# Kernel tuning notes

Hardware: AMD Instinct MI355X
Metric: run time of the kernel (lower is better)

Reference implementation:

```python
import jax, jax.numpy as jnp
import numpy as np

N_NODES = 50000
N_EDGES = 800000
N_GRAPHS = 64
IN_CH = 128
HID = 128
PROC_X = 128
Q_DIM = 768
PROC_Q = 128
OUT_CH = 32


def setup_inputs() -> dict:
    key = jax.random.key(0)
    ks = jax.random.split(key, 16)
    inp = {
        "x": jax.random.normal(ks[0], (N_NODES, IN_CH), dtype=jnp.float32),
        "edge_index": jax.random.randint(ks[1], (2, N_EDGES), 0, N_NODES, dtype=jnp.int64),
        "batch": jnp.sort(jax.random.randint(ks[2], (N_NODES,), 0, N_GRAPHS, dtype=jnp.int64)),
        "question_embedding": jax.random.normal(ks[3], (N_GRAPHS, Q_DIM), dtype=jnp.float32),
    }
    s = 1.0 / np.sqrt(HID)
    inp["W0"] = jax.random.uniform(ks[4], (IN_CH, HID), minval=-s, maxval=s)
    inp["b0"] = jnp.zeros((HID,), jnp.float32)
    inp["W1"] = jax.random.uniform(ks[5], (HID, HID), minval=-s, maxval=s)
    inp["b1"] = jnp.zeros((HID,), jnp.float32)
    inp["W2"] = jax.random.uniform(ks[6], (HID, PROC_X), minval=-s, maxval=s)
    inp["b2"] = jnp.zeros((PROC_X,), jnp.float32)
    inp["fc0_w"] = jax.random.uniform(ks[7], (Q_DIM, PROC_Q), minval=-s, maxval=s)
    inp["fc0_b"] = jnp.zeros((PROC_Q,), jnp.float32)
    inp["fc1_w"] = jax.random.uniform(ks[8], (PROC_X + PROC_Q, HID), minval=-s, maxval=s)
    inp["fc1_b"] = jnp.zeros((HID,), jnp.float32)
    inp["fc2_w"] = jax.random.uniform(ks[9], (HID, OUT_CH), minval=-s, maxval=s)
    inp["fc2_b"] = jnp.zeros((OUT_CH,), jnp.float32)
    return inp


def _gcn_norm(edge_index, n_nodes):
    """Add self-loops and compute symmetric GCN normalization per edge."""
    loop = jnp.arange(n_nodes, dtype=edge_index.dtype)
    src = jnp.concatenate([edge_index[0], loop])
    dst = jnp.concatenate([edge_index[1], loop])
    ones = jnp.ones_like(dst, dtype=jnp.float32)
    deg = jax.ops.segment_sum(ones, dst, num_segments=n_nodes)
    dinv = jnp.where(deg > 0, jax.lax.rsqrt(deg), 0.0)
    norm = dinv[src] * dinv[dst]  # [E+N]
    return src, dst, norm


def _gcn_conv(x, src, dst, norm, W, b):
    h = x @ W                                # [N, F_out]
    msg = h[src] * norm[:, None]             # gather + scale  [E+N, F_out]
    agg = jax.ops.segment_sum(msg, dst, num_segments=x.shape[0])
    return agg + b


def reference(x, edge_index, batch, question_embedding,
              W0, b0, W1, b1, W2, b2,
              fc0_w, fc0_b, fc1_w, fc1_b, fc2_w, fc2_b):
    n = x.shape[0]
    src, dst, norm = _gcn_norm(edge_index, n)
    h = jax.nn.relu(_gcn_conv(x, src, dst, norm, W0, b0))
    h = jax.nn.relu(_gcn_conv(h, src, dst, norm, W1, b1))
    h = jax.nn.relu(_gcn_conv(h, src, dst, norm, W2, b2))
    q = jax.nn.relu(question_embedding @ fc0_w + fc0_b)  # [G, PROC_Q]
    q_exp = q[batch]                                      # [N, PROC_Q]
    combined = jnp.concatenate([h, q_exp], axis=1)
    out = jax.nn.relu(combined @ fc1_w + fc1_b)
    out = out @ fc2_w + fc2_b
    return out
```

## Files before the change

### kernel.cpp

```cpp
#include <hip/hip_runtime.h>
#include <hip/hip_bf16.h>

#define N_NODES 50000
#define N_EDGES 800000
#define N_GRAPHS 64
#define LSTR 136

typedef __attribute__((ext_vector_type(4))) short s4v;
typedef __attribute__((ext_vector_type(8))) short s8v;
typedef __attribute__((ext_vector_type(16))) float f16v;

struct HL { short hi, lo; };

__device__ inline HL bsplit(float f) {
    HL r;
    unsigned u = __float_as_uint(f);
    unsigned rh = (u + 0x7FFFu + ((u >> 16) & 1u)) >> 16;
    r.hi = (short)rh;
    float fh = __uint_as_float(rh << 16);
    float fl = f - fh;
    unsigned u2 = __float_as_uint(fl);
    unsigned rl = (u2 + 0x7FFFu + ((u2 >> 16) & 1u)) >> 16;
    r.lo = (short)rl;
    return r;
}

__device__ inline unsigned short f2bf(float f) {
    unsigned u = __float_as_uint(f);
    return (unsigned short)((u + 0x7FFFu + ((u >> 16) & 1u)) >> 16);
}

__device__ inline float bflo(unsigned u) { return __uint_as_float(u << 16); }
__device__ inline float bfhi(unsigned u) { return __uint_as_float(u & 0xFFFF0000u); }

__device__ inline void gat8(const unsigned* __restrict__ Hs,
                            const unsigned short* __restrict__ colA,
                            int e, int l, float& a0, float& a1) {
    uint4 cw = *(const uint4*)(colA + e);
    unsigned u0 = Hs[(cw.x & 0xFFFFu) * 64u + l];
    unsigned u1 = Hs[(cw.x >> 16) * 64u + l];
    unsigned u2 = Hs[(cw.y & 0xFFFFu) * 64u + l];
    unsigned u3 = Hs[(cw.y >> 16) * 64u + l];
    unsigned u4 = Hs[(cw.z & 0xFFFFu) * 64u + l];
    unsigned u5 = Hs[(cw.z >> 16) * 64u + l];
    unsigned u6 = Hs[(cw.w & 0xFFFFu) * 64u + l];
    unsigned u7 = Hs[(cw.w >> 16) * 64u + l];
    a0 += ((bflo(u0) + bflo(u1)) + (bflo(u2) + bflo(u3)))
        + ((bflo(u4) + bflo(u5)) + (bflo(u6) + bflo(u7)));
    a1 += ((bfhi(u0) + bfhi(u1)) + (bfhi(u2) + bfhi(u3)))
        + ((bfhi(u4) + bfhi(u5)) + (bfhi(u6) + bfhi(u7)));
}


__global__ __launch_bounds__(512) void k_scan_a(const int* __restrict__ cnt,
                                                int* __restrict__ rowptr,
                                                int* __restrict__ bsum,
                                                float* __restrict__ dinv, int n) {
    __shared__ int s[512];
    int t = threadIdx.x;
    int i = blockIdx.x * 512 + t;
    int v = (i < n) ? cnt[i] : 0;
    if (i < n) dinv[i] = rsqrtf((float)(v + 1));
    int pv = (v + 7) & ~7;
    s[t] = pv;
    __syncthreads();
    for (int d = 1; d < 512; d <<= 1) {
        int x = (t >= d) ? s[t - d] : 0;
        __syncthreads();
        s[t] += x;
        __syncthreads();
    }
    if (i < n) rowptr[i] = s[t] - pv;
    if (t == 511) bsum[blockIdx.x] = s[511];
}

__global__ __launch_bounds__(512) void k_scan_c(int* __restrict__ rowptr,
                                                const int* __restrict__ bsum,
                                                int n, int nb) {
    __shared__ int sb[128];
    int t = threadIdx.x;
    if (t < 128) sb[t] = (t < nb) ? bsum[t] : 0;
    __syncthreads();
    for (int d = 1; d < 128; d <<= 1) {
        int x = 0;
        if (t < 128 && t >= d) x = sb[t - d];
        __syncthreads();
        if (t < 128) sb[t] += x;
        __syncthreads();
    }
    int add = (blockIdx.x > 0) ? sb[blockIdx.x - 1] : 0;
    int i = blockIdx.x * 512 + t;
    if (i < n) rowptr[i] += add;
    if (i == 0) rowptr[n] = sb[nb - 1];
}

__global__ __launch_bounds__(512) void k_prep(const float* __restrict__ qe,
                                              const float* __restrict__ fc0w,
                                              const float* __restrict__ fc0b,
                                              const float* __restrict__ fc1w,
                                              const float* __restrict__ fc1b,
                                              const float* __restrict__ W0,
                                              const float* __restrict__ W1,
                                              const float* __restrict__ W2,
                                              const float* __restrict__ fc2w,
                                              const int* __restrict__ ei,
                                              int* __restrict__ cnt,
                                              int* __restrict__ rank,
                                              short* __restrict__ WH,
                                              short* __restrict__ WL,
                                              unsigned* __restrict__ Hsd,
                                              unsigned short* __restrict__ colA,
                                              float* __restrict__ qq, int E) {
    int b = blockIdx.x, tid = threadIdx.x;
    if (b >= 482) {
        int e = (b - 482) * 512 + tid;
        if (e < E) rank[e] = atomicAdd(&cnt[ei[E + e]], 1);
        return;
    }
    if (b == 481) {
        if (tid < 64) Hsd[(unsigned)N_NODES * 64u + tid] = 0u;
        return;
    }
    if (b >= 200) {
        int idx = (b - 200) * 512 + tid;
        if (idx < 143752) {
            uint4 p;
            p.x = p.y = p.z = p.w = 0xC350C350u;
            ((uint4*)colA)[idx] = p;
        }
        return;
    }
    if (b >= 64) {
        int i = (b - 64) * 512 + tid;
        float val;
        int dst;
        if (i < 65536) {
            int mat = i >> 14, off = i & 16383;
            int k = off >> 7, n = off & 127;
            const float* src = (mat == 0) ? W0 : (mat == 1) ? W1 : (mat == 2) ? W2 : fc1w;
            val = src[k * 128 + n];
            dst = mat * 16384 + n * 128 + k;
        } else {
            int off = i - 65536;
            int k = off >> 5, n = off & 31;
            val = fc2w[k * 32 + n];
            dst = 65536 + n * 128 + k;
        }
        HL r = bsplit(val);
        WH[dst] = r.hi;
        WL[dst] = r.lo;
        return;
    }
    __shared__ float qs[768];
    __shared__ float red[512];
    __shared__ float ql[128];
    const float* fc1bot = fc1w + 128 * 128;
    int g = b;
    for (int i = tid; i < 768; i += 512) qs[i] = qe[g * 768 + i];
    __syncthreads();
    int j = tid & 127, sl = tid >> 7;
    int kb = sl * 192;
    float a0 = 0, a1 = 0, a2 = 0, a3 = 0;
    for (int k = 0; k < 192; k += 4) {
        a0 += qs[kb + k + 0] * fc0w[(kb + k + 0) * 128 + j];
        a1 += qs[kb + k + 1] * fc0w[(kb + k + 1) * 128 + j];
        a2 += qs[kb + k + 2] * fc0w[(kb + k + 2) * 128 + j];
        a3 += qs[kb + k + 3] * fc0w[(kb + k + 3) * 128 + j];
    }
    red[tid] = (a0 + a1) + (a2 + a3);
    __syncthreads();
    if (tid < 128)
        ql[tid] = fmaxf(((red[tid] + red[tid + 128]) + (red[tid + 256] + red[tid + 384]))
                        + fc0b[tid], 0.f);
    __syncthreads();
    kb = sl * 32;
    float b0 = 0, b1 = 0;
    for (int k = 0; k < 32; k += 2) {
        b0 += ql[kb + k + 0] * fc1bot[(kb + k + 0) * 128 + j];
        b1 += ql[kb + k + 1] * fc1bot[(kb + k + 1) * 128 + j];
    }
    red[tid] = b0 + b1;
    __syncthreads();
    if (tid < 128)
        qq[g * 128 + tid] = ((red[tid] + red[tid + 128]) + (red[tid + 256] + red[tid + 384]))
                            + fc1b[tid];
}

__global__ __launch_bounds__(128) void k_fg(const float* __restrict__ A32,
                                            const short* __restrict__ WTh,
                                            const short* __restrict__ WTl,
                                            const float* __restrict__ dinv,
                                            unsigned short* __restrict__ oHs,
                                            const int* __restrict__ ei,
                                            const int* __restrict__ rowptr,
                                            const int* __restrict__ rank,
                                            unsigned short* __restrict__ colA,
                                            int nrows, int E, int GG) {
    const int tid = threadIdx.x;
    if (blockIdx.x >= GG) {
        int e = (blockIdx.x - GG) * 128 + tid;
        if (e < E) colA[rowptr[ei[E + e]] + rank[e]] = (unsigned short)ei[e];
        return;
    }
    __shared__ short Ah[32 * LSTR];
    const int row0 = blockIdx.x * 32;

    #pragma unroll
    for (int i = 0; i < 8; ++i) {
        int u = i * 128 + tid;
        int r = u >> 5, c4 = u & 31;
        int gr = row0 + r;
        float4 v = make_float4(0.f, 0.f, 0.f, 0.f);
        if (gr < nrows) v = ((const float4*)A32)[(size_t)gr * 32 + c4];
        s4v h4 = {(short)f2bf(v.x), (short)f2bf(v.y), (short)f2bf(v.z), (short)f2bf(v.w)};
        *(s4v*)&Ah[r * LSTR + c4 * 4] = h4;
    }
    __syncthreads();

    const int wv = tid >> 6, lane = tid & 63;
    const int m = lane & 31, half = lane >> 5;
    const int c0 = wv * 64 + m;
    f16v acc0 = {0.f}, acc1 = {0.f};
    #pragma unroll
    for (int ks = 0; ks < 8; ++ks) {
        int ko = ks * 16 + half * 8;
        s8v ah  = *(const s8v*)&Ah[m * LSTR + ko];
        s8v bh0 = *(const s8v*)&WTh[(size_t)c0 * 128 + ko];
        s8v bl0 = *(const s8v*)&WTl[(size_t)c0 * 128 + ko];
        s8v bh1 = *(const s8v*)&WTh[(size_t)(c0 + 32) * 128 + ko];
        s8v bl1 = *(const s8v*)&WTl[(size_t)(c0 + 32) * 128 + ko];
        acc0 = __builtin_amdgcn_mfma_f32_32x32x16_bf16(ah, bh0, acc0, 0, 0, 0);
        acc0 = __builtin_amdgcn_mfma_f32_32x32x16_bf16(ah, bl0, acc0, 0, 0, 0);
        acc1 = __builtin_amdgcn_mfma_f32_32x32x16_bf16(ah, bh1, acc1, 0, 0, 0);
        acc1 = __builtin_amdgcn_mfma_f32_32x32x16_bf16(ah, bl1, acc1, 0, 0, 0);
    }

    #pragma unroll
    for (int reg = 0; reg < 16; ++reg) {
        int rl = (reg & 3) + 8 * (reg >> 2) + 4 * half;
        int gr = row0 + rl;
        if (gr >= nrows) continue;
        float sc = dinv[gr];
        oHs[(size_t)gr * 128 + c0]      = f2bf(acc0[reg] * sc);
        oHs[(size_t)gr * 128 + c0 + 32] = f2bf(acc1[reg] * sc);
    }
}

template <int FC>
__global__ __launch_bounds__(512) void k_gg(const unsigned* __restrict__ Hs,
                                            const int* __restrict__ rowptr,
                                            const unsigned short* __restrict__ colA,
                                            const float* __restrict__ dinv,
                                            const float* __restrict__ bias,
                                            const short* __restrict__ WTh,
                                            const short* __restrict__ WTl,
                                            const short* __restrict__ W2h,
                                            const short* __restrict__ W2l,
                                            const float* __restrict__ qq,
                                            const int* __restrict__ batch,
                                            const float* __restrict__ fc2b,
                                            unsigned short* __restrict__ oHs,
                                            float* __restrict__ out,
                                            int n) {
    __shared__ short Ah[32 * LSTR];
    __shared__ short Pl[FC ? 32 * LSTR : 1];
    __shared__ float red[FC ? 3 * 32 * 33 : 1];
    const int tid = threadIdx.x;
    const int row0 = blockIdx.x * 32;
    const int wv = tid >> 6, l = tid & 63;
    const int m = l & 31, half = l >> 5;

    const float2 bb = ((const float2*)bias)[l];
    for (int i = 0; i < 4; ++i) {
        int r = wv * 4 + i;
        int node = row0 + r;
        unsigned pack = 0;
        if (node < n) {
            int e0 = __builtin_amdgcn_readfirstlane(rowptr[node]);
            int e1 = __builtin_amdgcn_readfirstlane(rowptr[node + 1]);
            float a0 = 0.f, a1 = 0.f, c0v = 0.f, c1v = 0.f;
            int e = e0;
            for (; e + 16 <= e1; e += 16) {
                gat8(Hs, colA, e, l, a0, a1);
                gat8(Hs, colA, e + 8, l, c0v, c1v);
            }
            for (; e < e1; e += 8)
                gat8(Hs, colA, e, l, a0, a1);
            a0 += c0v;
            a1 += c1v;
            float di = dinv[node];
            unsigned uh = Hs[(unsigned)node * 64u + l];
            float o0 = fmaxf((a0 + bflo(uh)) * di + bb.x, 0.f);
            float o1 = fmaxf((a1 + bfhi(uh)) * di + bb.y, 0.f);
            pack = (unsigned)f2bf(o0) | ((unsigned)f2bf(o1) << 16);
        }
        ((unsigned*)Ah)[r * 68 + l] = pack;
    }
    __syncthreads();

    const int c0 = wv * 32 + m;
    f16v acc = {0.f};
    if (wv < 4) {
        #pragma unroll
        for (int ks = 0; ks < 8; ++ks) {
            int ko = ks * 16 + half * 8;
            s8v ah = *(const s8v*)&Ah[m * LSTR + ko];
            s8v bh = *(const s8v*)&WTh[(size_t)c0 * 128 + ko];
            s8v bl = *(const s8v*)&WTl[(size_t)c0 * 128 + ko];
            acc = __builtin_amdgcn_mfma_f32_32x32x16_bf16(ah, bh, acc, 0, 0, 0);
            acc = __builtin_amdgcn_mfma_f32_32x32x16_bf16(ah, bl, acc, 0, 0, 0);
        }
    }

    if (FC == 0) {
        if (wv < 4) {
            #pragma unroll
            for (int reg = 0; reg < 16; ++reg) {
                int rl = (reg & 3) + 8 * (reg >> 2) + 4 * half;
                int gr = row0 + rl;
                if (gr >= n) continue;
                oHs[(size_t)gr * 128 + c0] = f2bf(acc[reg] * dinv[gr]);
            }
        }
    } else {
        __syncthreads();
        if (wv < 4) {
            #pragma unroll
            for (int reg = 0; reg < 16; ++reg) {
                int rl = (reg & 3) + 8 * (reg >> 2) + 4 * half;
                int gr = row0 + rl;
                int g = (gr < n) ? batch[gr] : 0;
                float v = fmaxf(acc[reg] + qq[(size_t)g * 128 + c0], 0.f);
                HL p = bsplit(v);
                Ah[rl * LSTR + c0] = p.hi;
                Pl[rl * LSTR + c0] = p.lo;
            }
        }
        __syncthreads();
        f16v acc2 = {0.f};
        if (wv < 4) {
            #pragma unroll
            for (int ks = 0; ks < 2; ++ks) {
                int ko = wv * 32 + ks * 16 + half * 8;
                s8v ah = *(const s8v*)&Ah[m * LSTR + ko];
                s8v al = *(const s8v*)&Pl[m * LSTR + ko];
                s8v bh = *(const s8v*)&W2h[(size_t)m * 128 + ko];
                s8v bl = *(const s8v*)&W2l[(size_t)m * 128 + ko];
                acc2 = __builtin_amdgcn_mfma_f32_32x32x16_bf16(ah, bh, acc2, 0, 0, 0);
                acc2 = __builtin_amdgcn_mfma_f32_32x32x16_bf16(ah, bl, acc2, 0, 0, 0);
                acc2 = __builtin_amdgcn_mfma_f32_32x32x16_bf16(al, bh, acc2, 0, 0, 0);
            }
            if (wv > 0) {
                #pragma unroll
                for (int reg = 0; reg < 16; ++reg) {
                    int rl = (reg & 3) + 8 * (reg >> 2) + 4 * half;
                    red[(wv - 1) * 1056 + rl * 33 + m] = acc2[reg];
                }
            }
        }
        __syncthreads();
        if (wv == 0) {
            #pragma unroll
            for (int reg = 0; reg < 16; ++reg) {
                int rl = (reg & 3) + 8 * (reg >> 2) + 4 * half;
                int gr = row0 + rl;
                if (gr < n)
                    out[(size_t)gr * 32 + m] = acc2[reg]
                        + (red[rl * 33 + m] + red[1056 + rl * 33 + m])
                        + red[2112 + rl * 33 + m] + fc2b[m];
            }
        }
    }
}


extern "C" void kernel_launch(void* const* d_in, const int* in_sizes, int n_in,
                              void* d_out, int out_size, void* d_ws, size_t ws_size,
                              hipStream_t stream) {
    const float* x    = (const float*)d_in[0];
    const int*   ei   = (const int*)d_in[1];
    const int*   batch= (const int*)d_in[2];
    const float* qe   = (const float*)d_in[3];
    const float* W0   = (const float*)d_in[4];
    const float* b0   = (const float*)d_in[5];
    const float* W1   = (const float*)d_in[6];
    const float* b1   = (const float*)d_in[7];
    const float* W2   = (const float*)d_in[8];
    const float* b2   = (const float*)d_in[9];
    const float* fc0w = (const float*)d_in[10];
    const float* fc0b = (const float*)d_in[11];
    const float* fc1w = (const float*)d_in[12];
    const float* fc1b = (const float*)d_in[13];
    const float* fc2w = (const float*)d_in[14];
    const float* fc2b = (const float*)d_in[15];
    float* out = (float*)d_out;

    float* WS = (float*)d_ws;
    unsigned short* HS  = (unsigned short*)WS;
    unsigned short* HS2 = (unsigned short*)(WS + 3200064);
    float* DINV = WS + 6400128;
    float* QQ   = WS + 6450144;
    int*   CNT  = (int*)(WS + 6458336);
    int*   ROWPTR = (int*)(WS + 6508352);
    int*   RANK = (int*)(WS + 6558368);
    unsigned short* COL = (unsigned short*)(WS + 7358368);
    int*   BSUM = (int*)(WS + 7933376);
    short* WTH  = (short*)(WS + 7933504);
    short* WTL  = WTH + 69632;

    const int N = N_NODES, E = N_EDGES;
    const int sb = (N + 511) / 512;
    const int gg = (N + 31) / 32;
    const int histb = (E + 511) / 512;
    const int fillb = (E + 127) / 128;

    (void)hipMemsetAsync(CNT, 0, N * sizeof(int), stream);
    k_prep<<<482 + histb, 512, 0, stream>>>(qe, fc0w, fc0b, fc1w, fc1b,
                                            W0, W1, W2, fc2w, ei, CNT, RANK,
                                            WTH, WTL, (unsigned*)HS, COL, QQ, E);
    k_scan_a<<<sb, 512, 0, stream>>>(CNT, ROWPTR, BSUM, DINV, N);
    k_scan_c<<<sb, 512, 0, stream>>>(ROWPTR, BSUM, N, sb);
    k_fg<<<gg + fillb, 128, 0, stream>>>(x, WTH, WTL, DINV, HS,
                                         ei, ROWPTR, RANK, COL, N, E, gg);
    k_gg<0><<<gg, 512, 0, stream>>>((const unsigned*)HS, ROWPTR, COL, DINV, b0,
                                    WTH + 16384, WTL + 16384, nullptr, nullptr,
                                    nullptr, nullptr, nullptr, HS2, nullptr, N);
    k_gg<0><<<gg, 512, 0, stream>>>((const unsigned*)HS2, ROWPTR, COL, DINV, b1,
                                    WTH + 32768, WTL + 32768, nullptr, nullptr,
                                    nullptr, nullptr, nullptr, HS, nullptr, N);
    k_gg<1><<<gg, 512, 0, stream>>>((const unsigned*)HS, ROWPTR, COL, DINV, b2,
                                    WTH + 49152, WTL + 49152, WTH + 65536, WTL + 65536,
                                    QQ, batch, fc2b, nullptr, out, N);
}
```

Measured before the change: 310.0 us.

## Balance GCN gather across waves via edge-group ownership and shared atomics

The gather-GEMM kernel now spreads the padded 8-edge groups of a 32-row block evenly across 4 waves, instead of giving each wave fixed rows. A per-group row-label array, written during CSR fill, tells each group which row to add into, and partial sums are combined with LDS atomics. The gather loop is software-pipelined two groups ahead, and blocks shrink from 512 to 256 threads so all waves do MFMA work. The goal is to remove load imbalance from skewed degrees and to raise occupancy, at the cost of LDS atomic traffic and an extra byte array that reuses the count buffer.

```diff
diff --git a/kernel.cpp b/kernel.cpp
--- a/kernel.cpp
+++ b/kernel.cpp
@@ -32,24 +32,6 @@
 
 __device__ inline float bflo(unsigned u) { return __uint_as_float(u << 16); }
 __device__ inline float bfhi(unsigned u) { return __uint_as_float(u & 0xFFFF0000u); }
-
-__device__ inline void gat8(const unsigned* __restrict__ Hs,
-                            const unsigned short* __restrict__ colA,
-                            int e, int l, float& a0, float& a1) {
-    uint4 cw = *(const uint4*)(colA + e);
-    unsigned u0 = Hs[(cw.x & 0xFFFFu) * 64u + l];
-    unsigned u1 = Hs[(cw.x >> 16) * 64u + l];
-    unsigned u2 = Hs[(cw.y & 0xFFFFu) * 64u + l];
-    unsigned u3 = Hs[(cw.y >> 16) * 64u + l];
-    unsigned u4 = Hs[(cw.z & 0xFFFFu) * 64u + l];
-    unsigned u5 = Hs[(cw.z >> 16) * 64u + l];
-    unsigned u6 = Hs[(cw.w & 0xFFFFu) * 64u + l];
-    unsigned u7 = Hs[(cw.w >> 16) * 64u + l];
-    a0 += ((bflo(u0) + bflo(u1)) + (bflo(u2) + bflo(u3)))
-        + ((bflo(u4) + bflo(u5)) + (bflo(u6) + bflo(u7)));
-    a1 += ((bfhi(u0) + bfhi(u1)) + (bfhi(u2) + bfhi(u3)))
-        + ((bfhi(u4) + bfhi(u5)) + (bfhi(u6) + bfhi(u7)));
-}
 
 
 __global__ __launch_bounds__(512) void k_scan_a(const int* __restrict__ cnt,
@@ -119,6 +101,7 @@
     }
     if (b == 481) {
         if (tid < 64) Hsd[(unsigned)N_NODES * 64u + tid] = 0u;
+        if (tid >= 64 && tid < 128) Hsd[100001u * 64u + (unsigned)(tid - 64)] = 0u;
         return;
     }
     if (b >= 200) {
@@ -195,11 +178,18 @@
                                             const int* __restrict__ rowptr,
                                             const int* __restrict__ rank,
                                             unsigned short* __restrict__ colA,
+                                            unsigned char* __restrict__ grpl,
                                             int nrows, int E, int GG) {
     const int tid = threadIdx.x;
     if (blockIdx.x >= GG) {
         int e = (blockIdx.x - GG) * 128 + tid;
-        if (e < E) colA[rowptr[ei[E + e]] + rank[e]] = (unsigned short)ei[e];
+        if (e < E) {
+            int dst = ei[E + e];
+            int rk = rank[e];
+            int pos = rowptr[dst] + rk;
+            colA[pos] = (unsigned short)ei[e];
+            if ((rk & 7) == 0) grpl[pos >> 3] = (unsigned char)(dst & 31);
+        }
         return;
     }
     __shared__ short Ah[32 * LSTR];
@@ -247,115 +237,160 @@
 }
 
 template <int FC>
-__global__ __launch_bounds__(512) void k_gg(const unsigned* __restrict__ Hs,
-                                            const int* __restrict__ rowptr,
-                                            const unsigned short* __restrict__ colA,
-                                            const float* __restrict__ dinv,
-                                            const float* __restrict__ bias,
-                                            const short* __restrict__ WTh,
-                                            const short* __restrict__ WTl,
-                                            const short* __restrict__ W2h,
-                                            const short* __restrict__ W2l,
-                                            const float* __restrict__ qq,
-                                            const int* __restrict__ batch,
-                                            const float* __restrict__ fc2b,
-                                            unsigned short* __restrict__ oHs,
-                                            float* __restrict__ out,
-                                            int n) {
-    __shared__ short Ah[32 * LSTR];
-    __shared__ short Pl[FC ? 32 * LSTR : 1];
-    __shared__ float red[FC ? 3 * 32 * 33 : 1];
+__global__ __launch_bounds__(256, 7) void k_gg(const unsigned* __restrict__ Hs,
+                                               const int* __restrict__ rowptr,
+                                               const unsigned short* __restrict__ colA,
+                                               const unsigned char* __restrict__ grpl,
+                                               const float* __restrict__ dinv,
+                                               const float* __restrict__ bias,
+                                               const short* __restrict__ WTh,
+                                               const short* __restrict__ WTl,
+                                               const short* __restrict__ W2h,
+                                               const short* __restrict__ W2l,
+                                               const float* __restrict__ qq,
+                                               const int* __restrict__ batch,
+                                               const float* __restrict__ fc2b,
+                                               unsigned short* __restrict__ oHs,
+                                               float* __restrict__ out,
+                                               int n) {
+    __shared__ __align__(16) char SMraw[17408];
+    float* acc = (float*)SMraw;
+    short* Ah  = (short*)SMraw;
     const int tid = threadIdx.x;
     const int row0 = blockIdx.x * 32;
     const int wv = tid >> 6, l = tid & 63;
     const int m = l & 31, half = l >> 5;
 
-    const float2 bb = ((const float2*)bias)[l];
-    for (int i = 0; i < 4; ++i) {
-        int r = wv * 4 + i;
-        int node = row0 + r;
-        unsigned pack = 0;
-        if (node < n) {
-            int e0 = __builtin_amdgcn_readfirstlane(rowptr[node]);
-            int e1 = __builtin_amdgcn_readfirstlane(rowptr[node + 1]);
-            float a0 = 0.f, a1 = 0.f, c0v = 0.f, c1v = 0.f;
-            int e = e0;
-            for (; e + 16 <= e1; e += 16) {
-                gat8(Hs, colA, e, l, a0, a1);
-                gat8(Hs, colA, e + 8, l, c0v, c1v);
-            }
-            for (; e < e1; e += 8)
-                gat8(Hs, colA, e, l, a0, a1);
-            a0 += c0v;
-            a1 += c1v;
-            float di = dinv[node];
-            unsigned uh = Hs[(unsigned)node * 64u + l];
-            float o0 = fmaxf((a0 + bflo(uh)) * di + bb.x, 0.f);
-            float o1 = fmaxf((a1 + bfhi(uh)) * di + bb.y, 0.f);
-            pack = (unsigned)f2bf(o0) | ((unsigned)f2bf(o1) << 16);
-        }
-        ((unsigned*)Ah)[r * 68 + l] = pack;
+    #pragma unroll
+    for (int i = 0; i < 4; ++i)
+        ((float4*)acc)[i * 256 + tid] = make_float4(0.f, 0.f, 0.f, 0.f);
+    __syncthreads();
+
+    const int rend = (row0 + 32 < n) ? (row0 + 32) : n;
+    const unsigned g0 = (unsigned)(rowptr[row0] >> 3);
+    const unsigned g1 = (unsigned)(rowptr[rend] >> 3);
+    const int ng = (int)(g1 - g0);
+    int cntw = ng - wv;
+    cntw = (cntw > 0) ? ((cntw + 3) >> 2) : 0;
+
+    if (cntw > 0) {
+        unsigned gA = g0 + (unsigned)wv;
+        uint4 cwA = *(const uint4*)(colA + (size_t)gA * 8);
+        int rA = (int)grpl[gA];
+        unsigned gBq = (cntw > 1) ? (gA + 4u) : gA;
+        uint4 cwB = *(const uint4*)(colA + (size_t)gBq * 8);
+        int rB = (int)grpl[gBq];
+        unsigned a0 = Hs[(cwA.x & 0xFFFFu) * 64u + l];
+        unsigned a1 = Hs[(cwA.x >> 16) * 64u + l];
+        unsigned a2 = Hs[(cwA.y & 0xFFFFu) * 64u + l];
+        unsigned a3 = Hs[(cwA.y >> 16) * 64u + l];
+        unsigned a4 = Hs[(cwA.z & 0xFFFFu) * 64u + l];
+        unsigned a5 = Hs[(cwA.z >> 16) * 64u + l];
+        unsigned a6 = Hs[(cwA.w & 0xFFFFu) * 64u + l];
+        unsigned a7 = Hs[(cwA.w >> 16) * 64u + l];
+        for (int k = 0; k < cntw; ++k) {
+            unsigned gCq = (k + 2 < cntw) ? (gA + 8u) : gA;
+            uint4 cwC = *(const uint4*)(colA + (size_t)gCq * 8);
+            int rC = (int)grpl[gCq];
+            unsigned b0 = Hs[(cwB.x & 0xFFFFu) * 64u + l];
+            unsigned b1 = Hs[(cwB.x >> 16) * 64u + l];
+            unsigned b2 = Hs[(cwB.y & 0xFFFFu) * 64u + l];
+            unsigned b3 = Hs[(cwB.y >> 16) * 64u + l];
+            unsigned b4 = Hs[(cwB.z & 0xFFFFu) * 64u + l];
+            unsigned b5 = Hs[(cwB.z >> 16) * 64u + l];
+            unsigned b6 = Hs[(cwB.w & 0xFFFFu) * 64u + l];
+            unsigned b7 = Hs[(cwB.w >> 16) * 64u + l];
+            float slo = ((bflo(a0) + bflo(a1)) + (bflo(a2) + bflo(a3)))
+                      + ((bflo(a4) + bflo(a5)) + (bflo(a6) + bflo(a7)));
+            float shi = ((bfhi(a0) + bfhi(a1)) + (bfhi(a2) + bfhi(a3)))
+                      + ((bfhi(a4) + bfhi(a5)) + (bfhi(a6) + bfhi(a7)));
+            atomicAdd(&acc[(rA << 7) + l], slo);
+            atomicAdd(&acc[(rA << 7) + 64 + l], shi);
+            a0 = b0; a1 = b1; a2 = b2; a3 = b3;
+            a4 = b4; a5 = b5; a6 = b6; a7 = b7;
+            rA = rB; cwB = cwC; rB = rC; gA += 4u;
+        }
+    }
+    __syncthreads();
+
+    unsigned pk[8];
+    #pragma unroll
+    for (int i = 0; i < 8; ++i) {
+        int item = i * 256 + tid;
+        int r = item >> 6, lc = item & 63;
+        int gr = row0 + r;
+        bool alive = gr < n;
+        float lo = acc[(r << 7) + lc];
+        float hi = acc[(r << 7) + 64 + lc];
+        unsigned su = Hs[(unsigned)(alive ? gr : N_NODES) * 64u + lc];
+        float di = dinv[alive ? gr : (n - 1)];
+        float2 bb = ((const float2*)bias)[lc];
+        float o0 = fmaxf((lo + bflo(su)) * di + bb.x, 0.f);
+        float o1 = fmaxf((hi + bfhi(su)) * di + bb.y, 0.f);
+        pk[i] = alive ? ((unsigned)f2bf(o0) | ((unsigned)f2bf(o1) << 16)) : 0u;
+    }
+    __syncthreads();
+    #pragma unroll
+    for (int i = 0; i < 8; ++i) {
+        int item = i * 256 + tid;
+        int r = item >> 6, lc = item & 63;
+        ((unsigned*)Ah)[r * 68 + lc] = pk[i];
     }
     __syncthreads();
 
     const int c0 = wv * 32 + m;
-    f16v acc = {0.f};
-    if (wv < 4) {
+    f16v fa = {0.f};
+    #pragma unroll
+    for (int ks = 0; ks < 8; ++ks) {
+        int ko = ks * 16 + half * 8;
+        s8v ah = *(const s8v*)&Ah[m * LSTR + ko];
+        s8v bh = *(const s8v*)&WTh[(size_t)c0 * 128 + ko];
+        s8v bl = *(const s8v*)&WTl[(size_t)c0 * 128 + ko];
+        fa = __builtin_amdgcn_mfma_f32_32x32x16_bf16(ah, bh, fa, 0, 0, 0);
+        fa = __builtin_amdgcn_mfma_f32_32x32x16_bf16(ah, bl, fa, 0, 0, 0);
+    }
+
+    if (FC == 0) {
         #pragma unroll
-        for (int ks = 0; ks < 8; ++ks) {
-            int ko = ks * 16 + half * 8;
+        for (int reg = 0; reg < 16; ++reg) {
+            int rl = (reg & 3) + 8 * (reg >> 2) + 4 * half;
+            int gr = row0 + rl;
+            if (gr >= n) continue;
+            oHs[(size_t)gr * 128 + c0] = f2bf(fa[reg] * dinv[gr]);
+        }
+    } else {
+        short* Pl = Ah + 32 * LSTR;
+        __syncthreads();
+        #pragma unroll
+        for (int reg = 0; reg < 16; ++reg) {
+            int rl = (reg & 3) + 8 * (reg >> 2) + 4 * half;
+            int gr = row0 + rl;
+            int g = (gr < n) ? batch[gr] : 0;
+            float v = fmaxf(fa[reg] + qq[(size_t)g * 128 + c0], 0.f);
+            HL p = bsplit(v);
+            Ah[rl * LSTR + c0] = p.hi;
+            Pl[rl * LSTR + c0] = p.lo;
+        }
+        __syncthreads();
+        f16v acc2 = {0.f};
+        #pragma unroll
+        for (int ks = 0; ks < 2; ++ks) {
+            int ko = wv * 32 + ks * 16 + half * 8;
             s8v ah = *(const s8v*)&Ah[m * LSTR + ko];
-            s8v bh = *(const s8v*)&WTh[(size_t)c0 * 128 + ko];
-            s8v bl = *(const s8v*)&WTl[(size_t)c0 * 128 + ko];
-            acc = __builtin_amdgcn_mfma_f32_32x32x16_bf16(ah, bh, acc, 0, 0, 0);
-            acc = __builtin_amdgcn_mfma_f32_32x32x16_bf16(ah, bl, acc, 0, 0, 0);
-        }
-    }
-
-    if (FC == 0) {
-        if (wv < 4) {
+            s8v al = *(const s8v*)&Pl[m * LSTR + ko];
+            s8v bh = *(const s8v*)&W2h[(size_t)m * 128 + ko];
+            s8v bl = *(const s8v*)&W2l[(size_t)m * 128 + ko];
+            acc2 = __builtin_amdgcn_mfma_f32_32x32x16_bf16(ah, bh, acc2, 0, 0, 0);
+            acc2 = __builtin_amdgcn_mfma_f32_32x32x16_bf16(ah, bl, acc2, 0, 0, 0);
+            acc2 = __builtin_amdgcn_mfma_f32_32x32x16_bf16(al, bh, acc2, 0, 0, 0);
+        }
+        __syncthreads();
+        float* red = (float*)SMraw;
+        if (wv > 0) {
             #pragma unroll
             for (int reg = 0; reg < 16; ++reg) {
                 int rl = (reg & 3) + 8 * (reg >> 2) + 4 * half;
-                int gr = row0 + rl;
-                if (gr >= n) continue;
-                oHs[(size_t)gr * 128 + c0] = f2bf(acc[reg] * dinv[gr]);
-            }
-        }
-    } else {
-        __syncthreads();
-        if (wv < 4) {
-            #pragma unroll
-            for (int reg = 0; reg < 16; ++reg) {
-                int rl = (reg & 3) + 8 * (reg >> 2) + 4 * half;
-                int gr = row0 + rl;
-                int g = (gr < n) ? batch[gr] : 0;
-                float v = fmaxf(acc[reg] + qq[(size_t)g * 128 + c0], 0.f);
-                HL p = bsplit(v);
-                Ah[rl * LSTR + c0] = p.hi;
-                Pl[rl * LSTR + c0] = p.lo;
-            }
-        }
-        __syncthreads();
-        f16v acc2 = {0.f};
-        if (wv < 4) {
-            #pragma unroll
-            for (int ks = 0; ks < 2; ++ks) {
-                int ko = wv * 32 + ks * 16 + half * 8;
-                s8v ah = *(const s8v*)&Ah[m * LSTR + ko];
-                s8v al = *(const s8v*)&Pl[m * LSTR + ko];
-                s8v bh = *(const s8v*)&W2h[(size_t)m * 128 + ko];
-                s8v bl = *(const s8v*)&W2l[(size_t)m * 128 + ko];
-                acc2 = __builtin_amdgcn_mfma_f32_32x32x16_bf16(ah, bh, acc2, 0, 0, 0);
-                acc2 = __builtin_amdgcn_mfma_f32_32x32x16_bf16(ah, bl, acc2, 0, 0, 0);
-                acc2 = __builtin_amdgcn_mfma_f32_32x32x16_bf16(al, bh, acc2, 0, 0, 0);
-            }
-            if (wv > 0) {
-                #pragma unroll
-                for (int reg = 0; reg < 16; ++reg) {
-                    int rl = (reg & 3) + 8 * (reg >> 2) + 4 * half;
-                    red[(wv - 1) * 1056 + rl * 33 + m] = acc2[reg];
-                }
+                red[(wv - 1) * 1056 + rl * 33 + m] = acc2[reg];
             }
         }
         __syncthreads();
@@ -407,6 +442,7 @@
     int*   BSUM = (int*)(WS + 7933376);
     short* WTH  = (short*)(WS + 7933504);
     short* WTL  = WTH + 69632;
+    unsigned char* GRPL = (unsigned char*)CNT;
 
     const int N = N_NODES, E = N_EDGES;
     const int sb = (N + 511) / 512;
@@ -421,14 +457,14 @@
     k_scan_a<<<sb, 512, 0, stream>>>(CNT, ROWPTR, BSUM, DINV, N);
     k_scan_c<<<sb, 512, 0, stream>>>(ROWPTR, BSUM, N, sb);
     k_fg<<<gg + fillb, 128, 0, stream>>>(x, WTH, WTL, DINV, HS,
-                                         ei, ROWPTR, RANK, COL, N, E, gg);
-    k_gg<0><<<gg, 512, 0, stream>>>((const unsigned*)HS, ROWPTR, COL, DINV, b0,
+                                         ei, ROWPTR, RANK, COL, GRPL, N, E, gg);
+    k_gg<0><<<gg, 256, 0, stream>>>((const unsigned*)HS, ROWPTR, COL, GRPL, DINV, b0,
                                     WTH + 16384, WTL + 16384, nullptr, nullptr,
                                     nullptr, nullptr, nullptr, HS2, nullptr, N);
-    k_gg<0><<<gg, 512, 0, stream>>>((const unsigned*)HS2, ROWPTR, COL, DINV, b1,
+    k_gg<0><<<gg, 256, 0, stream>>>((const unsigned*)HS2, ROWPTR, COL, GRPL, DINV, b1,
                                     WTH + 32768, WTL + 32768, nullptr, nullptr,
                                     nullptr, nullptr, nullptr, HS, nullptr, N);
-    k_gg<1><<<gg, 512, 0, stream>>>((const unsigned*)HS, ROWPTR, COL, DINV, b2,
+    k_gg<1><<<gg, 256, 0, stream>>>((const unsigned*)HS, ROWPTR, COL, GRPL, DINV, b2,
                                     WTH + 49152, WTL + 49152, WTH + 65536, WTL + 65536,
                                     QQ, batch, fc2b, nullptr, out, N);
 }
```

Result: slower. 482.2 us (+55.6%).
